# Performance work log

Measured on AMD Instinct MI355X. Metric: run time of the kernel, lower is better.

Reference implementation:

```python
import jax, jax.numpy as jnp
import numpy as np

T, B, E, H = 1024, 8, 1024, 16
DH = E // H
MASKED_BIAS = -10000.0


def setup_inputs() -> dict:
    key = jax.random.key(0)
    k1, k2, k3 = jax.random.split(key, 3)
    query = jax.random.normal(k1, (T, B, E), dtype=jnp.float32)
    # xavier-uniform-ish scale for the fused QKV and output projections
    qkv_w = jax.random.normal(k2, (3 * E, E), dtype=jnp.float32) * (1.0 / np.sqrt(2.0 * E))
    out_w = jax.random.normal(k3, (E, E), dtype=jnp.float32) * (1.0 / np.sqrt(E))
    return {
        "query": query,
        "qkv_w": qkv_w,
        "qkv_b": jnp.zeros((3 * E,), jnp.float32),
        "out_w": out_w,
        "out_b": jnp.zeros((E,), jnp.float32),
    }


def reference(query, qkv_w, qkv_b, out_w, out_b):
    # query: [T, B, E] (Time x Batch x Channel, fairseq convention)
    tgt_len, bsz, embed_dim = query.shape
    scaling = DH ** (-0.5)

    # Fused QKV projection (QuantLinear fake-quant treated as identity numerics)
    qkv = jnp.einsum("tbe,fe->tbf", query, qkv_w) + qkv_b  # [T, B, 3E]
    q, k, v = jnp.split(qkv, 3, axis=-1)
    q = q * scaling

    def to_heads(x):  # [T, B, E] -> [B*H, T, DH]
        return x.reshape(tgt_len, bsz * H, DH).transpose(1, 0, 2)

    q, k, v = to_heads(q), to_heads(k), to_heads(v)

    # attn_weights: [B*H, T, S]
    attn_weights = jnp.einsum("ntd,nsd->nts", q, k)

    # causal mask from the tril `bias` buffer with masked_bias fill
    causal = jnp.tril(jnp.ones((tgt_len, tgt_len), dtype=bool))
    attn_weights = jnp.where(causal[None, :, :], attn_weights,
                             jnp.asarray(MASKED_BIAS, attn_weights.dtype))

    attn_probs = jax.nn.softmax(attn_weights, axis=-1)
    # dropout p=0.0 in eval: no-op

    attn = jnp.einsum("nts,nsd->ntd", attn_probs, v)  # [B*H, T, DH]
    attn = attn.transpose(1, 0, 2).reshape(tgt_len, bsz, embed_dim)  # [T, B, E]

    out = jnp.einsum("tbe,fe->tbf", attn, out_w) + out_b
    return out
```

## Files before the change

### kernel.cpp

```cpp
#include <hip/hip_runtime.h>

typedef __attribute__((ext_vector_type(4))) float f32x4;
typedef __attribute__((ext_vector_type(16))) float f32x16;
typedef __attribute__((ext_vector_type(8))) short bf16x8;
typedef __attribute__((ext_vector_type(4))) unsigned short u16x4;
typedef __attribute__((ext_vector_type(4))) unsigned int u32x4;

#define T_DIM 1024
#define B_DIM 8
#define E_DIM 1024
#define H_DIM 16
#define DH 64

__device__ __forceinline__ unsigned short f2bf(float f) {
  unsigned int u = __builtin_bit_cast(unsigned int, f);
  u += 0x7fffu + ((u >> 16) & 1u);
  return (unsigned short)(u >> 16);
}

__device__ __forceinline__ unsigned int cvtpk_bf16(float lo, float hi) {
  unsigned int r;
  asm("v_cvt_pk_bf16_f32 %0, %1, %2" : "=v"(r) : "v"(lo), "v"(hi));
  return r;
}

__device__ __forceinline__ float exp2_hw(float x) {
  float r;
  asm("v_exp_f32 %0, %1" : "=v"(r) : "v"(x));
  return r;
}

__device__ __forceinline__ f32x4 mfma16(bf16x8 a, bf16x8 b, f32x4 c) {
  return __builtin_amdgcn_mfma_f32_16x16x32_bf16(a, b, c, 0, 0, 0);
}
__device__ __forceinline__ f32x16 mfma32(bf16x8 a, bf16x8 b, f32x16 c) {
  return __builtin_amdgcn_mfma_f32_32x32x16_bf16(a, b, c, 0, 0, 0);
}

__global__ __launch_bounds__(256) void cast_f32_to_bf16(
    const float* __restrict__ src, unsigned short* __restrict__ dst, int n4) {
  int i = blockIdx.x * 256 + threadIdx.x;
  if (i >= n4) return;
  f32x4 v = *(const f32x4*)(src + (size_t)i * 4);
  u16x4 o;
  o[0] = f2bf(v[0]); o[1] = f2bf(v[1]); o[2] = f2bf(v[2]); o[3] = f2bf(v[3]);
  *(u16x4*)(dst + (size_t)i * 4) = o;
}

__device__ __forceinline__ void mainloop_128x256(
    const unsigned short* __restrict__ Ab,
    const unsigned short* __restrict__ Bb,
    unsigned short* smem, f32x4 acc[4][4]) {
  const int tid = threadIdx.x;
  const int wave = tid >> 6, lane = tid & 63;
  const int lr = lane & 15, lg = lane >> 4;
  const int x7 = lr & 7;
  const int wr = wave >> 2, wc = wave & 3;
  const int rlo = lane >> 3;
  const int csw = 8 * ((lane & 7) ^ rlo);

#define STG(KT, BUF)                                                            \
  {                                                                             \
    unsigned short* la_ = smem + (BUF) * 24576;                                 \
    unsigned short* lb_ = la_ + 8192;                                           \
    _Pragma("unroll")                                                           \
    for (int c_ = 0; c_ < 2; ++c_) {                                            \
      const int ins_ = wave * 2 + c_;                                           \
      __builtin_amdgcn_global_load_lds(                                         \
          (const __attribute__((address_space(1))) void*)(Ab + (size_t)(ins_ * 8 + rlo) * 1024 + (KT) * 64 + csw), \
          (__attribute__((address_space(3))) void*)(la_ + ins_ * 512), 16, 0, 0); \
    }                                                                           \
    _Pragma("unroll")                                                           \
    for (int c_ = 0; c_ < 4; ++c_) {                                            \
      const int ins_ = wave * 4 + c_;                                           \
      __builtin_amdgcn_global_load_lds(                                         \
          (const __attribute__((address_space(1))) void*)(Bb + (size_t)(ins_ * 8 + rlo) * 1024 + (KT) * 64 + csw), \
          (__attribute__((address_space(3))) void*)(lb_ + ins_ * 512), 16, 0, 0); \
    }                                                                           \
  }

#define COMPUTE(BUF)                                                            \
  {                                                                             \
    const unsigned short* la_ = smem + (BUF) * 24576;                           \
    const unsigned short* ha_ = la_ + (wr * 64) * 64;                           \
    const unsigned short* hb_ = la_ + 8192 + (wc * 64) * 64;                    \
    _Pragma("unroll")                                                           \
    for (int ks_ = 0; ks_ < 2; ++ks_) {                                         \
      bf16x8 af_[4], bf_[4];                                                    \
      const int cu_ = (((ks_ * 4 + lg) ^ x7) << 3);                             \
      _Pragma("unroll")                                                         \
      for (int i_ = 0; i_ < 4; ++i_) {                                          \
        af_[i_] = *(const bf16x8*)(ha_ + (i_ * 16 + lr) * 64 + cu_);            \
        bf_[i_] = *(const bf16x8*)(hb_ + (i_ * 16 + lr) * 64 + cu_);            \
      }                                                                         \
      __builtin_amdgcn_s_setprio(1);                                            \
      _Pragma("unroll")                                                         \
      for (int mi_ = 0; mi_ < 4; ++mi_)                                         \
        _Pragma("unroll")                                                       \
        for (int ni_ = 0; ni_ < 4; ++ni_)                                       \
          acc[mi_][ni_] = mfma16(af_[mi_], bf_[ni_], acc[mi_][ni_]);            \
      __builtin_amdgcn_s_setprio(0);                                            \
    }                                                                           \
  }

#define ENDT(WAITSTR)                                                           \
  asm volatile("s_waitcnt " WAITSTR ::: "memory");                              \
  __builtin_amdgcn_s_barrier();                                                 \
  __builtin_amdgcn_sched_barrier(0);

  STG(0, 0) STG(1, 1)
  ENDT("vmcnt(6)")

  for (int tt = 0; tt < 12; tt += 3) {
    STG(tt + 2, 2) COMPUTE(0) ENDT("vmcnt(6)")
    STG(tt + 3, 0) COMPUTE(1) ENDT("vmcnt(6)")
    STG(tt + 4, 1) COMPUTE(2) ENDT("vmcnt(6)")
  }
  STG(14, 2) COMPUTE(0) ENDT("vmcnt(6)")
  STG(15, 0) COMPUTE(1) ENDT("vmcnt(6)")
  COMPUTE(2) ENDT("vmcnt(0)")
  COMPUTE(0)
#undef STG
#undef COMPUTE
#undef ENDT
}

__global__ __launch_bounds__(512) void gemm_qkv9(
    const unsigned short* __restrict__ A, const unsigned short* __restrict__ W,
    const float* __restrict__ bias,
    unsigned short* __restrict__ Qh, unsigned short* __restrict__ Kh,
    unsigned short* __restrict__ Vh) {
  extern __shared__ unsigned short smem[];
  const int bid = blockIdx.x;
  const int swz = (bid & 7) * 96 + (bid >> 3);
  const int m0 = (swz & 63) * 128;
  const int n0 = (swz >> 6) * 256;

  f32x4 acc[4][4];
  const f32x4 z4 = {0.f, 0.f, 0.f, 0.f};
#pragma unroll
  for (int i = 0; i < 4; ++i)
#pragma unroll
    for (int j = 0; j < 4; ++j) acc[i][j] = z4;

  mainloop_128x256(A + (size_t)m0 * 1024, W + (size_t)n0 * 1024, smem, acc);

  const int lane = threadIdx.x & 63, wave = threadIdx.x >> 6;
  const int lr = lane & 15, lg = lane >> 4;
  const int wr = wave >> 2, wc = wave & 3;
#pragma unroll
  for (int mf = 0; mf < 4; ++mf)
#pragma unroll
    for (int nf = 0; nf < 4; ++nf)
#pragma unroll
      for (int j = 0; j < 4; ++j) {
        int m = m0 + wr * 64 + mf * 16 + lg * 4 + j;
        int f = n0 + wc * 64 + nf * 16 + lr;
        float v = acc[mf][nf][j] + bias[f];
        int t = m >> 3, b = m & 7;
        int e = f & 1023, h = e >> 6, d = e & 63;
        int which = f >> 10;
        size_t idx = ((size_t)(b * 16 + h) * T_DIM + t) * DH + d;
        if (which == 0)      Qh[idx] = f2bf(v * 0.18033688011111772f);
        else if (which == 1) Kh[idx] = f2bf(v);
        else                 Vh[idx] = f2bf(v);
      }
}

__global__ __launch_bounds__(512) void gemm_out9(
    const unsigned short* __restrict__ A, const unsigned short* __restrict__ W,
    const float* __restrict__ bias, float* __restrict__ out) {
  extern __shared__ unsigned short smem[];
  const int bid = blockIdx.x;
  const int swz = (bid & 7) * 32 + (bid >> 3);
  const int m0 = (swz & 63) * 128;
  const int n0 = (swz >> 6) * 256;

  f32x4 acc[4][4];
  const f32x4 z4 = {0.f, 0.f, 0.f, 0.f};
#pragma unroll
  for (int i = 0; i < 4; ++i)
#pragma unroll
    for (int j = 0; j < 4; ++j) acc[i][j] = z4;

  mainloop_128x256(A + (size_t)m0 * 1024, W + (size_t)n0 * 1024, smem, acc);

  const int lane = threadIdx.x & 63, wave = threadIdx.x >> 6;
  const int lr = lane & 15, lg = lane >> 4;
  const int wr = wave >> 2, wc = wave & 3;
#pragma unroll
  for (int mf = 0; mf < 4; ++mf)
#pragma unroll
    for (int nf = 0; nf < 4; ++nf)
#pragma unroll
      for (int j = 0; j < 4; ++j) {
        int m = m0 + wr * 64 + mf * 16 + lg * 4 + j;
        int f = n0 + wc * 64 + nf * 16 + lr;
        out[(size_t)m * E_DIM + f] = acc[mf][nf][j] + bias[f];
      }
}

__global__ __launch_bounds__(256) void transpose_v(
    const unsigned short* __restrict__ Vh, unsigned short* __restrict__ Vt) {
  __shared__ unsigned short tile[64][72];
  const int n = blockIdx.x, t0 = blockIdx.y * 64;
  const int tid = threadIdx.x;
  const int r = tid >> 3, c8 = tid & 7;
#pragma unroll
  for (int it = 0; it < 2; ++it) {
    int row = it * 32 + r;
    bf16x8 v = *(const bf16x8*)(Vh + ((size_t)n * T_DIM + t0 + row) * DH + c8 * 8);
    *(bf16x8*)&tile[row][c8 * 8] = v;
  }
  __syncthreads();
#pragma unroll
  for (int it = 0; it < 2; ++it) {
    int d = it * 32 + r;
    bf16x8 ov;
#pragma unroll
    for (int jj = 0; jj < 8; ++jj) ov[jj] = (short)tile[c8 * 8 + jj][d];
    *(bf16x8*)(Vt + ((size_t)n * DH + d) * T_DIM + t0 + c8 * 8) = ov;
  }
}

__global__ __launch_bounds__(256) void flash_attn6(
    const unsigned short* __restrict__ Qh, const unsigned short* __restrict__ Kh,
    const unsigned short* __restrict__ Vt, unsigned short* __restrict__ attn) {
  __shared__ unsigned short lds[2][2][4096];
  const int tid = threadIdx.x;
  const int wave = tid >> 6, lane = tid & 63;
  const int lq = lane & 31, hi = lane >> 5;
  const int bid = blockIdx.x;
  const int qt = 7 - (bid >> 7);
  const int n = bid & 127;
  const int b = n >> 4, h = n & 15;
  const int q0w = qt * 128 + wave * 32;
  const int q = q0w + lq;
  const int nbb = 2 * qt + 2;
  const int mynb = (q0w + 95) >> 6;

  const unsigned short* kh_n = Kh + (size_t)n * (T_DIM * DH);
  const unsigned short* vt_n = Vt + (size_t)n * (DH * T_DIM);

  const int rlo = lane >> 3;
  const int csw = 8 * ((lane & 7) ^ rlo);

#define STAGE(S0, BUF)                                                          \
  {                                                                             \
    _Pragma("unroll")                                                           \
    for (int m_ = 0; m_ < 2; ++m_) {                                            \
      const int instr_ = wave * 2 + m_;                                         \
      const int r_ = instr_ * 8 + rlo;                                          \
      __builtin_amdgcn_global_load_lds(                                         \
          (const __attribute__((address_space(1))) void*)(kh_n + (size_t)((S0) + r_) * DH + csw), \
          (__attribute__((address_space(3))) void*)(&lds[BUF][0][instr_ * 512]), 16, 0, 0); \
      __builtin_amdgcn_global_load_lds(                                         \
          (const __attribute__((address_space(1))) void*)(vt_n + (size_t)r_ * T_DIM + (S0) + csw), \
          (__attribute__((address_space(3))) void*)(&lds[BUF][1][instr_ * 512]), 16, 0, 0); \
    }                                                                           \
  }

  bf16x8 qf[4];
  const unsigned short* qp = Qh + ((size_t)n * T_DIM + q) * DH + hi * 8;
#pragma unroll
  for (int kk = 0; kk < 4; ++kk) qf[kk] = *(const bf16x8*)(qp + kk * 16);

  f32x16 o0, o1;
#pragma unroll
  for (int r = 0; r < 16; ++r) { o0[r] = 0.f; o1[r] = 0.f; }
  float m_run = -1e30f, l_run = 0.f;

  STAGE(0, 0);
  asm volatile("s_waitcnt vmcnt(0)");
  __builtin_amdgcn_s_barrier();

  const int swzr = (lq & 7) << 4;

  for (int i = 0; i < nbb; ++i) {
    const int cur = i & 1;
    if (i + 1 < nbb) {
      STAGE((i + 1) * 64, cur ^ 1);
      asm volatile("s_waitcnt vmcnt(4)");
    } else {
      asm volatile("s_waitcnt vmcnt(0)");
    }
    __builtin_amdgcn_s_barrier();
    __builtin_amdgcn_sched_barrier(0);

    if (i < mynb) {
      const int s0 = i * 64;
      const unsigned short* kb = lds[cur][0];
      const unsigned short* vb = lds[cur][1];
      f32x16 sA, sB;
#pragma unroll
      for (int r = 0; r < 16; ++r) { sA[r] = 0.f; sB[r] = 0.f; }
      __builtin_amdgcn_s_setprio(1);
#pragma unroll
      for (int kk = 0; kk < 4; ++kk) {
        const int cb = ((kk * 32 + hi * 16) ^ swzr) >> 1;
        bf16x8 ka = *(const bf16x8*)(kb + lq * 64 + cb);
        bf16x8 kbf = *(const bf16x8*)(kb + (32 + lq) * 64 + cb);
        sA = mfma32(ka, qf[kk], sA);
        sB = mfma32(kbf, qf[kk], sB);
      }
      __builtin_amdgcn_s_setprio(0);
      if (i == mynb - 1) {
#pragma unroll
        for (int r = 0; r < 16; ++r) {
          int sp = s0 + (r & 3) + 8 * (r >> 2) + 4 * hi;
          if (sp > q)      sA[r] = -10000.0f;
          if (sp + 32 > q) sB[r] = -10000.0f;
        }
      }
      float t0 = fmaxf(sA[0], sB[0]), t1 = fmaxf(sA[1], sB[1]);
      float t2 = fmaxf(sA[2], sB[2]), t3 = fmaxf(sA[3], sB[3]);
#pragma unroll
      for (int r = 4; r < 16; r += 4) {
        t0 = fmaxf(t0, fmaxf(sA[r], sB[r]));
        t1 = fmaxf(t1, fmaxf(sA[r + 1], sB[r + 1]));
        t2 = fmaxf(t2, fmaxf(sA[r + 2], sB[r + 2]));
        t3 = fmaxf(t3, fmaxf(sA[r + 3], sB[r + 3]));
      }
      float tmax = fmaxf(fmaxf(t0, t1), fmaxf(t2, t3));
      tmax = fmaxf(tmax, __shfl_xor(tmax, 32));
      if (__any(tmax - m_run > 11.5f)) {
        float m_new = fmaxf(m_run, tmax);
        float sc = exp2_hw(m_run - m_new);
        l_run *= sc;
#pragma unroll
        for (int r = 0; r < 16; ++r) { o0[r] *= sc; o1[r] *= sc; }
        m_run = m_new;
      }
      float r0 = 0.f, r1 = 0.f, r2 = 0.f, r3 = 0.f;
#pragma unroll
      for (int r = 0; r < 16; r += 4) {
        sA[r] = exp2_hw(sA[r] - m_run);         r0 += sA[r];
        sA[r + 1] = exp2_hw(sA[r + 1] - m_run); r1 += sA[r + 1];
        sA[r + 2] = exp2_hw(sA[r + 2] - m_run); r2 += sA[r + 2];
        sA[r + 3] = exp2_hw(sA[r + 3] - m_run); r3 += sA[r + 3];
      }
#pragma unroll
      for (int r = 0; r < 16; r += 4) {
        sB[r] = exp2_hw(sB[r] - m_run);         r0 += sB[r];
        sB[r + 1] = exp2_hw(sB[r + 1] - m_run); r1 += sB[r + 1];
        sB[r + 2] = exp2_hw(sB[r + 2] - m_run); r2 += sB[r + 2];
        sB[r + 3] = exp2_hw(sB[r + 3] - m_run); r3 += sB[r + 3];
      }
      float rs = (r0 + r1) + (r2 + r3);
      rs += __shfl_xor(rs, 32);
      l_run += rs;
      unsigned int pk[16];
#pragma unroll
      for (int ii = 0; ii < 8; ++ii) pk[ii]     = cvtpk_bf16(sA[2 * ii], sA[2 * ii + 1]);
#pragma unroll
      for (int ii = 0; ii < 8; ++ii) pk[8 + ii] = cvtpk_bf16(sB[2 * ii], sB[2 * ii + 1]);
      __builtin_amdgcn_s_setprio(1);
#pragma unroll
      for (int ks = 0; ks < 4; ++ks) {
        unsigned int A0 = pk[ks * 4 + 0], A1 = pk[ks * 4 + 1];
        unsigned int B0 = pk[ks * 4 + 2], B1 = pk[ks * 4 + 3];
        unsigned int xA0 = __shfl_xor(A0, 32), xA1 = __shfl_xor(A1, 32);
        unsigned int xB0 = __shfl_xor(B0, 32), xB1 = __shfl_xor(B1, 32);
        u32x4 uu;
        uu[0] = hi ? xB0 : A0;
        uu[1] = hi ? xB1 : A1;
        uu[2] = hi ? B0 : xA0;
        uu[3] = hi ? B1 : xA1;
        bf16x8 pf = __builtin_bit_cast(bf16x8, uu);
        const int cb = ((ks * 32 + hi * 16) ^ swzr) >> 1;
        bf16x8 v0 = *(const bf16x8*)(vb + lq * 64 + cb);
        bf16x8 v1 = *(const bf16x8*)(vb + (32 + lq) * 64 + cb);
        o0 = mfma32(v0, pf, o0);
        o1 = mfma32(v1, pf, o1);
      }
      __builtin_amdgcn_s_setprio(0);
    }
    __builtin_amdgcn_s_barrier();
  }
#undef STAGE

  const float inv = 1.0f / l_run;
  unsigned short* op = attn + ((size_t)q * B_DIM + b) * E_DIM + h * DH;
#pragma unroll
  for (int g = 0; g < 4; ++g) {
    u16x4 w0, w1;
#pragma unroll
    for (int jj = 0; jj < 4; ++jj) {
      w0[jj] = f2bf(o0[g * 4 + jj] * inv);
      w1[jj] = f2bf(o1[g * 4 + jj] * inv);
    }
    int d = 8 * g + 4 * hi;
    *(u16x4*)(op + d) = w0;
    *(u16x4*)(op + 32 + d) = w1;
  }
}

extern "C" void kernel_launch(void* const* d_in, const int* in_sizes, int n_in,
                              void* d_out, int out_size, void* d_ws, size_t ws_size,
                              hipStream_t stream) {
  const float* query = (const float*)d_in[0];
  const float* qkv_w = (const float*)d_in[1];
  const float* qkv_b = (const float*)d_in[2];
  const float* out_w = (const float*)d_in[3];
  const float* out_b = (const float*)d_in[4];
  float* out = (float*)d_out;

  char* ws = (char*)d_ws;
  unsigned short* Abf  = (unsigned short*)(ws);
  unsigned short* Wbf  = (unsigned short*)(ws + (size_t)(16u << 20));
  unsigned short* OWbf = (unsigned short*)(ws + (size_t)(22u << 20));
  unsigned short* Qh   = (unsigned short*)(ws + (size_t)(24u << 20));
  unsigned short* Kh   = (unsigned short*)(ws + (size_t)(40u << 20));
  unsigned short* Vh   = (unsigned short*)(ws + (size_t)(56u << 20));
  unsigned short* Vt   = (unsigned short*)(ws + (size_t)(72u << 20));
  unsigned short* attn = Abf;

  cast_f32_to_bf16<<<8192, 256, 0, stream>>>(query, Abf, 8388608 / 4);
  cast_f32_to_bf16<<<3072, 256, 0, stream>>>(qkv_w, Wbf, 3145728 / 4);
  cast_f32_to_bf16<<<1024, 256, 0, stream>>>(out_w, OWbf, 1048576 / 4);
  gemm_qkv9<<<768, 512, 147456, stream>>>(Abf, Wbf, qkv_b, Qh, Kh, Vh);
  transpose_v<<<dim3(128, 16), 256, 0, stream>>>(Vh, Vt);
  flash_attn6<<<1024, 256, 0, stream>>>(Qh, Kh, Vt, attn);
  gemm_out9<<<256, 512, 147456, stream>>>(attn, OWbf, out_b, out);
}
```

Baseline: 161.3 us.

## Shrink GEMM tiles to 128x128 with 4 waves and double buffering

Both projection GEMMs move from a 128x256 tile with 8 waves and triple-buffered dynamic LDS to a 128x128 tile with 4 waves, two static LDS buffers and a simple syncthreads pipeline. This doubles the block count (1536 and 512) to fill the CUs better, and the smaller LDS footprint allows more resident blocks per CU. In exchange, each tile reuses its operands less and the shallower pipeline with full barriers may leave load latency exposed.

```diff
diff --git a/kernel.cpp b/kernel.cpp
--- a/kernel.cpp
+++ b/kernel.cpp
@@ -47,7 +47,7 @@
   *(u16x4*)(dst + (size_t)i * 4) = o;
 }
 
-__device__ __forceinline__ void mainloop_128x256(
+__device__ __forceinline__ void mainloop_128x128(
     const unsigned short* __restrict__ Ab,
     const unsigned short* __restrict__ Bb,
     unsigned short* smem, f32x4 acc[4][4]) {
@@ -55,25 +55,21 @@
   const int wave = tid >> 6, lane = tid & 63;
   const int lr = lane & 15, lg = lane >> 4;
   const int x7 = lr & 7;
-  const int wr = wave >> 2, wc = wave & 3;
+  const int wr = wave >> 1, wc = wave & 1;
   const int rlo = lane >> 3;
   const int csw = 8 * ((lane & 7) ^ rlo);
 
 #define STG(KT, BUF)                                                            \
   {                                                                             \
-    unsigned short* la_ = smem + (BUF) * 24576;                                 \
+    unsigned short* la_ = smem + (BUF) * 16384;                                 \
     unsigned short* lb_ = la_ + 8192;                                           \
-    _Pragma("unroll")                                                           \
-    for (int c_ = 0; c_ < 2; ++c_) {                                            \
-      const int ins_ = wave * 2 + c_;                                           \
-      __builtin_amdgcn_global_load_lds(                                         \
-          (const __attribute__((address_space(1))) void*)(Ab + (size_t)(ins_ * 8 + rlo) * 1024 + (KT) * 64 + csw), \
-          (__attribute__((address_space(3))) void*)(la_ + ins_ * 512), 16, 0, 0); \
-    }                                                                           \
     _Pragma("unroll")                                                           \
     for (int c_ = 0; c_ < 4; ++c_) {                                            \
       const int ins_ = wave * 4 + c_;                                           \
       __builtin_amdgcn_global_load_lds(                                         \
+          (const __attribute__((address_space(1))) void*)(Ab + (size_t)(ins_ * 8 + rlo) * 1024 + (KT) * 64 + csw), \
+          (__attribute__((address_space(3))) void*)(la_ + ins_ * 512), 16, 0, 0); \
+      __builtin_amdgcn_global_load_lds(                                         \
           (const __attribute__((address_space(1))) void*)(Bb + (size_t)(ins_ * 8 + rlo) * 1024 + (KT) * 64 + csw), \
           (__attribute__((address_space(3))) void*)(lb_ + ins_ * 512), 16, 0, 0); \
     }                                                                           \
@@ -81,7 +77,7 @@
 
 #define COMPUTE(BUF)                                                            \
   {                                                                             \
-    const unsigned short* la_ = smem + (BUF) * 24576;                           \
+    const unsigned short* la_ = smem + (BUF) * 16384;                           \
     const unsigned short* ha_ = la_ + (wr * 64) * 64;                           \
     const unsigned short* hb_ = la_ + 8192 + (wc * 64) * 64;                    \
     _Pragma("unroll")                                                           \
@@ -103,38 +99,28 @@
     }                                                                           \
   }
 
-#define ENDT(WAITSTR)                                                           \
-  asm volatile("s_waitcnt " WAITSTR ::: "memory");                              \
-  __builtin_amdgcn_s_barrier();                                                 \
-  __builtin_amdgcn_sched_barrier(0);
-
-  STG(0, 0) STG(1, 1)
-  ENDT("vmcnt(6)")
-
-  for (int tt = 0; tt < 12; tt += 3) {
-    STG(tt + 2, 2) COMPUTE(0) ENDT("vmcnt(6)")
-    STG(tt + 3, 0) COMPUTE(1) ENDT("vmcnt(6)")
-    STG(tt + 4, 1) COMPUTE(2) ENDT("vmcnt(6)")
-  }
-  STG(14, 2) COMPUTE(0) ENDT("vmcnt(6)")
-  STG(15, 0) COMPUTE(1) ENDT("vmcnt(6)")
-  COMPUTE(2) ENDT("vmcnt(0)")
-  COMPUTE(0)
+  STG(0, 0)
+  __syncthreads();
+#pragma unroll 4
+  for (int t = 0; t < 16; ++t) {
+    if (t < 15) STG(t + 1, (t + 1) & 1)
+    COMPUTE(t & 1)
+    __syncthreads();
+  }
 #undef STG
 #undef COMPUTE
-#undef ENDT
-}
-
-__global__ __launch_bounds__(512) void gemm_qkv9(
+}
+
+__global__ __launch_bounds__(256) void gemm_qkv10(
     const unsigned short* __restrict__ A, const unsigned short* __restrict__ W,
     const float* __restrict__ bias,
     unsigned short* __restrict__ Qh, unsigned short* __restrict__ Kh,
     unsigned short* __restrict__ Vh) {
-  extern __shared__ unsigned short smem[];
+  __shared__ unsigned short smem[32768];
   const int bid = blockIdx.x;
-  const int swz = (bid & 7) * 96 + (bid >> 3);
+  const int swz = (bid & 7) * 192 + (bid >> 3);
   const int m0 = (swz & 63) * 128;
-  const int n0 = (swz >> 6) * 256;
+  const int n0 = (swz >> 6) * 128;
 
   f32x4 acc[4][4];
   const f32x4 z4 = {0.f, 0.f, 0.f, 0.f};
@@ -143,11 +129,11 @@
 #pragma unroll
     for (int j = 0; j < 4; ++j) acc[i][j] = z4;
 
-  mainloop_128x256(A + (size_t)m0 * 1024, W + (size_t)n0 * 1024, smem, acc);
+  mainloop_128x128(A + (size_t)m0 * 1024, W + (size_t)n0 * 1024, smem, acc);
 
   const int lane = threadIdx.x & 63, wave = threadIdx.x >> 6;
   const int lr = lane & 15, lg = lane >> 4;
-  const int wr = wave >> 2, wc = wave & 3;
+  const int wr = wave >> 1, wc = wave & 1;
 #pragma unroll
   for (int mf = 0; mf < 4; ++mf)
 #pragma unroll
@@ -167,14 +153,14 @@
       }
 }
 
-__global__ __launch_bounds__(512) void gemm_out9(
+__global__ __launch_bounds__(256) void gemm_out10(
     const unsigned short* __restrict__ A, const unsigned short* __restrict__ W,
     const float* __restrict__ bias, float* __restrict__ out) {
-  extern __shared__ unsigned short smem[];
+  __shared__ unsigned short smem[32768];
   const int bid = blockIdx.x;
-  const int swz = (bid & 7) * 32 + (bid >> 3);
+  const int swz = (bid & 7) * 64 + (bid >> 3);
   const int m0 = (swz & 63) * 128;
-  const int n0 = (swz >> 6) * 256;
+  const int n0 = (swz >> 6) * 128;
 
   f32x4 acc[4][4];
   const f32x4 z4 = {0.f, 0.f, 0.f, 0.f};
@@ -183,11 +169,11 @@
 #pragma unroll
     for (int j = 0; j < 4; ++j) acc[i][j] = z4;
 
-  mainloop_128x256(A + (size_t)m0 * 1024, W + (size_t)n0 * 1024, smem, acc);
+  mainloop_128x128(A + (size_t)m0 * 1024, W + (size_t)n0 * 1024, smem, acc);
 
   const int lane = threadIdx.x & 63, wave = threadIdx.x >> 6;
   const int lr = lane & 15, lg = lane >> 4;
-  const int wr = wave >> 2, wc = wave & 3;
+  const int wr = wave >> 1, wc = wave & 1;
 #pragma unroll
   for (int mf = 0; mf < 4; ++mf)
 #pragma unroll
@@ -418,8 +404,8 @@
   cast_f32_to_bf16<<<8192, 256, 0, stream>>>(query, Abf, 8388608 / 4);
   cast_f32_to_bf16<<<3072, 256, 0, stream>>>(qkv_w, Wbf, 3145728 / 4);
   cast_f32_to_bf16<<<1024, 256, 0, stream>>>(out_w, OWbf, 1048576 / 4);
-  gemm_qkv9<<<768, 512, 147456, stream>>>(Abf, Wbf, qkv_b, Qh, Kh, Vh);
+  gemm_qkv10<<<1536, 256, 0, stream>>>(Abf, Wbf, qkv_b, Qh, Kh, Vh);
   transpose_v<<<dim3(128, 16), 256, 0, stream>>>(Vh, Vt);
   flash_attn6<<<1024, 256, 0, stream>>>(Qh, Kh, Vt, attn);
-  gemm_out9<<<256, 512, 147456, stream>>>(attn, OWbf, out_b, out);
-}
+  gemm_out10<<<512, 256, 0, stream>>>(attn, OWbf, out_b, out);
+}
```

Result: slower. 169.9 us (+5.3%).
